# Kernel optimization log

Measured on AMD Instinct MI355X. Metric: run time of the kernel, lower is better.

The kernel has to match this reference:

```python
import jax, jax.numpy as jnp
import numpy as np

N_HEADS = 16


def setup_inputs() -> dict:
    key = jax.random.key(0)
    ks = jax.random.split(key, 4)
    B, S, D = 2, 2048, 1024
    x = jax.random.normal(ks[0], (B, S, D), dtype=jnp.float32)
    scale = 1.0 / np.sqrt(D)
    Wq = jax.random.normal(ks[1], (D, D), dtype=jnp.float32) * scale
    Wk = jax.random.normal(ks[2], (D, D), dtype=jnp.float32) * scale
    Wv = jax.random.normal(ks[3], (D, D), dtype=jnp.float32) * scale
    bq = jnp.zeros((D,), jnp.float32)
    bk = jnp.zeros((D,), jnp.float32)
    bv = jnp.zeros((D,), jnp.float32)
    return {"x": x, "Wq": Wq, "bq": bq, "Wk": Wk, "bk": bk, "Wv": Wv, "bv": bv}


def _split_heads(t, n_heads):
    B, S, D = t.shape
    return t.reshape(B, S, n_heads, D // n_heads).transpose(0, 2, 1, 3)  # [B,H,S,hd]


def reference(x, Wq, bq, Wk, bk, Wv, bv):
    H = N_HEADS
    Q = _split_heads(x @ Wq + bq, H)
    K = _split_heads(x @ Wk + bk, H)
    V = _split_heads(x @ Wv + bv, H)
    head_size = Q.shape[-1]
    scores = jnp.einsum("bhqd,bhkd->bhqk", Q, K) / jnp.sqrt(jnp.float32(head_size))
    probs = jax.nn.softmax(scores, axis=-1)  # dropout p=0.01 -> identity in eval
    out = jnp.einsum("bhqk,bhkd->bhqd", probs, V)
    B, _, S, hd = out.shape
    return out.transpose(0, 2, 1, 3).reshape(B, S, H * hd)
```

## Files before the change

kernel.cpp:

```cpp
#include <hip/hip_runtime.h>
#include <hip/hip_bf16.h>

typedef __bf16 bf16x8 __attribute__((ext_vector_type(8)));
typedef __bf16 bf16x4 __attribute__((ext_vector_type(4)));
typedef float f32x4 __attribute__((ext_vector_type(4)));

#define B_ 2
#define S_ 2048
#define D_ 1024
#define H_ 16
#define HD_ 64
#define NT_ (S_ / 64)

__device__ inline void load_lds16(const __bf16* g, __bf16* l) {
  __builtin_amdgcn_global_load_lds(
      (const __attribute__((address_space(1))) void*)g,
      (__attribute__((address_space(3))) void*)l, 16, 0, 0);
}

__global__ __launch_bounds__(256) void prep(
    const float* __restrict__ X,
    const float* __restrict__ Wq, const float* __restrict__ Wk,
    const float* __restrict__ Wv,
    __bf16* __restrict__ Xb, __bf16* __restrict__ WT)
{
  const int z = blockIdx.z, t = threadIdx.x;
  if (z == 3) {
    size_t base = ((size_t)(blockIdx.y * 16 + blockIdx.x)) * 16384 + t * 4;
#pragma unroll
    for (int i = 0; i < 16; ++i) {
      size_t idx = base + (size_t)i * 1024;
      f32x4 v = *(const f32x4*)(X + idx);
      __bf16 o[4];
#pragma unroll
      for (int j = 0; j < 4; ++j) o[j] = (__bf16)v[j];
      *(ulong1*)(Xb + idx) = *(ulong1*)o;
    }
    return;
  }
  const float* W = (z == 0) ? Wq : (z == 1) ? Wk : Wv;
  __bf16* WTz = WT + (size_t)z * D_ * D_;
  const int k0 = blockIdx.y * 64, n0 = blockIdx.x * 64;

  __shared__ __bf16 T[64 * 72];
  {
    int kl = t >> 2, cg = (t & 3) * 16;
    const float* wp = W + (size_t)(k0 + kl) * D_ + n0 + cg;
    bf16x8 a, b;
#pragma unroll
    for (int j = 0; j < 4; ++j) { a[j] = (__bf16)wp[j];     a[4 + j] = (__bf16)wp[4 + j]; }
#pragma unroll
    for (int j = 0; j < 4; ++j) { b[j] = (__bf16)wp[8 + j]; b[4 + j] = (__bf16)wp[12 + j]; }
    *(bf16x8*)(T + kl * 72 + cg) = a;
    *(bf16x8*)(T + kl * 72 + cg + 8) = b;
  }
  __syncthreads();
  {
    int nl = t >> 2, kc = (t & 3) * 16;
    bf16x8 a, b;
#pragma unroll
    for (int j = 0; j < 8; ++j) a[j] = T[(kc + j) * 72 + nl];
#pragma unroll
    for (int j = 0; j < 8; ++j) b[j] = T[(kc + 8 + j) * 72 + nl];
    __bf16* op = WTz + (size_t)(n0 + nl) * D_ + k0 + kc;
    *(bf16x8*)(op) = a;
    *(bf16x8*)(op + 8) = b;
  }
}

__global__ __launch_bounds__(256) void qkv_gemm(
    const __bf16* __restrict__ Xb, const __bf16* __restrict__ WT,
    const float* __restrict__ bq, const float* __restrict__ bk,
    const float* __restrict__ bv,
    __bf16* __restrict__ Qw, __bf16* __restrict__ Kw, __bf16* __restrict__ VTw)
{
  const int z = blockIdx.z;
  const __bf16* Wz = WT + (size_t)z * D_ * D_;
  const float* bias = (z == 0) ? bq : (z == 1) ? bk : bv;
  __bf16* outp = (z == 0) ? Qw : (z == 1) ? Kw : VTw;
  const float mult = (z == 0) ? 0.125f * 1.44269504088896f : 1.0f;

  const int tid  = threadIdx.x;
  const int wave = tid >> 6, lane = tid & 63, ln = lane & 15, quad = lane >> 4;
  const int m0 = blockIdx.y * 128, n0 = blockIdx.x * 128;
  const int wm = (wave & 1) * 64, wn = (wave >> 1) * 64;

  __shared__ __bf16 Als[128 * 32];
  __shared__ __bf16 Bls[128 * 32];

  f32x4 acc[4][4] = {};

  for (int k0 = 0; k0 < D_; k0 += 32) {
    __syncthreads();
#pragma unroll
    for (int i = 0; i < 2; ++i) {
      int cb = wave * 128 + i * 64;
      int chunk = cb + lane;
      int row = chunk >> 2, c = chunk & 3;
      int gc = c ^ (row & 3);
      load_lds16(Xb + (size_t)(m0 + row) * D_ + k0 + gc * 8, Als + cb * 8);
      load_lds16(Wz + (size_t)(n0 + row) * D_ + k0 + gc * 8, Bls + cb * 8);
    }
    __syncthreads();

    bf16x8 af[4], bfr[4];
    const int dsw = (quad ^ (ln & 3)) * 8;
#pragma unroll
    for (int mt = 0; mt < 4; ++mt)
      af[mt] = *(const bf16x8*)(Als + (wm + mt * 16 + ln) * 32 + dsw);
#pragma unroll
    for (int nt = 0; nt < 4; ++nt)
      bfr[nt] = *(const bf16x8*)(Bls + (wn + nt * 16 + ln) * 32 + dsw);
#pragma unroll
    for (int mt = 0; mt < 4; ++mt)
#pragma unroll
      for (int nt = 0; nt < 4; ++nt)
        acc[mt][nt] = __builtin_amdgcn_mfma_f32_16x16x32_bf16(af[mt], bfr[nt], acc[mt][nt], 0, 0, 0);
  }

#pragma unroll
  for (int nt = 0; nt < 4; ++nt) {
    int n_g = n0 + wn + nt * 16 + ln;
    float bv_ = bias[n_g];
#pragma unroll
    for (int mt = 0; mt < 4; ++mt) {
      if (z < 2) {
#pragma unroll
        for (int r = 0; r < 4; ++r) {
          int m_g = m0 + wm + mt * 16 + quad * 4 + r;
          outp[(size_t)m_g * D_ + n_g] = (__bf16)((acc[mt][nt][r] + bv_) * mult);
        }
      } else {
        int m_g0 = m0 + wm + mt * 16 + quad * 4;
        bf16x4 v4;
#pragma unroll
        for (int r = 0; r < 4; ++r) v4[r] = (__bf16)(acc[mt][nt][r] + bv_);
        *(bf16x4*)(outp + (size_t)(m_g0 >> 11) * D_ * S_ + (size_t)n_g * S_ + (m_g0 & (S_ - 1))) = v4;
      }
    }
  }
}

__global__ __launch_bounds__(256) void attn(
    const __bf16* __restrict__ Q, const __bf16* __restrict__ K,
    const __bf16* __restrict__ VT, float* __restrict__ out)
{
  const int tid  = threadIdx.x;
  const int wave = tid >> 6, lane = tid & 63, ln = lane & 15, quad = lane >> 4;

  const int f = blockIdx.x;
  const int xcd = f & 7, g = f >> 3;
  const int bh = ((g & 3) << 3) | xcd;
  const int qt = g >> 2;
  const int b = bh >> 4, h = bh & 15;
  const int q0 = qt * 128 + wave * 32;

  const __bf16* Qbase = Q + (size_t)(b * S_ + q0) * D_ + h * HD_;
  bf16x8 qb[2][2];
#pragma unroll
  for (int nt = 0; nt < 2; ++nt)
#pragma unroll
    for (int ks = 0; ks < 2; ++ks)
      qb[nt][ks] = *(const bf16x8*)(Qbase + (size_t)(nt * 16 + ln) * D_ + ks * 32 + quad * 8);

  const __bf16* Kh = K + (size_t)b * S_ * D_ + h * HD_;
  const __bf16* Vh = VT + (size_t)(b * D_ + h * HD_) * S_;

  __shared__ __bf16 Kls[2][64 * 64];
  __shared__ __bf16 Vls[2][80 * 64];
  __shared__ __bf16 Pls[4][32 * 64];
  __bf16* Pw = Pls[wave];

  {
    bf16x8 ones;
#pragma unroll
    for (int j = 0; j < 8; ++j) ones[j] = (__bf16)1.0f;
    int buf = tid >> 7, rr = (tid >> 3) & 15, cc = tid & 7;
    *(bf16x8*)(&Vls[buf][(64 + rr) * 64 + cc * 8]) = ones;
  }

  f32x4 acc[2][5] = {};

  const int swl = ln & 7;

  bf16x8 kreg[2], vreg[2];
#pragma unroll
  for (int i = 0; i < 2; ++i) {
    int chunk = i * 256 + tid, row = chunk >> 3, cc = chunk & 7;
    kreg[i] = *(const bf16x8*)(Kh + (size_t)row * D_ + cc * 8);
    vreg[i] = *(const bf16x8*)(Vh + (size_t)row * S_ + cc * 8);
  }

  for (int kt = 0; kt < NT_; ++kt) {
    __bf16* Kb = Kls[kt & 1];
    __bf16* Vb = Vls[kt & 1];
#pragma unroll
    for (int i = 0; i < 2; ++i) {
      int chunk = i * 256 + tid, row = chunk >> 3, cc = chunk & 7;
      int sw = (cc ^ (row & 7)) * 8;
      *(bf16x8*)(Kb + row * 64 + sw) = kreg[i];
      *(bf16x8*)(Vb + row * 64 + sw) = vreg[i];
    }
    if (kt + 1 < NT_) {
#pragma unroll
      for (int i = 0; i < 2; ++i) {
        int chunk = i * 256 + tid, row = chunk >> 3, cc = chunk & 7;
        kreg[i] = *(const bf16x8*)(Kh + (size_t)((kt + 1) * 64 + row) * D_ + cc * 8);
        vreg[i] = *(const bf16x8*)(Vh + (size_t)row * S_ + (kt + 1) * 64 + cc * 8);
      }
    }
    __syncthreads();

    f32x4 st[4][2] = {};
#pragma unroll
    for (int mt = 0; mt < 4; ++mt) {
#pragma unroll
      for (int ks = 0; ks < 2; ++ks) {
        bf16x8 ka = *(const bf16x8*)(Kb + (mt * 16 + ln) * 64 + ((ks * 4 + quad) ^ swl) * 8);
#pragma unroll
        for (int nt = 0; nt < 2; ++nt)
          st[mt][nt] = __builtin_amdgcn_mfma_f32_16x16x32_bf16(ka, qb[nt][ks], st[mt][nt], 0, 0, 0);
      }
    }

#pragma unroll
    for (int mt = 0; mt < 4; ++mt)
#pragma unroll
      for (int nt = 0; nt < 2; ++nt) {
        bf16x4 pk;
#pragma unroll
        for (int r = 0; r < 4; ++r)
          pk[r] = (__bf16)__builtin_amdgcn_exp2f(st[mt][nt][r]);
        *(bf16x4*)(Pw + (nt * 16 + ln) * 64 + ((2 * mt + (quad >> 1)) ^ swl) * 8 + (quad & 1) * 4) = pk;
      }

#pragma unroll
    for (int ks = 0; ks < 2; ++ks) {
      bf16x8 pa[2];
#pragma unroll
      for (int mt = 0; mt < 2; ++mt)
        pa[mt] = *(const bf16x8*)(Pw + (mt * 16 + ln) * 64 + ((ks * 4 + quad) ^ swl) * 8);
#pragma unroll
      for (int dt = 0; dt < 5; ++dt) {
        int vrow = (dt < 4) ? dt * 16 + ln : 64 + ln;
        bf16x8 vb = *(const bf16x8*)(Vb + vrow * 64 + ((ks * 4 + quad) ^ swl) * 8);
#pragma unroll
        for (int mt = 0; mt < 2; ++mt)
          acc[mt][dt] = __builtin_amdgcn_mfma_f32_16x16x32_bf16(pa[mt], vb, acc[mt][dt], 0, 0, 0);
      }
    }
    __syncthreads();
  }

#pragma unroll
  for (int mt = 0; mt < 2; ++mt)
#pragma unroll
    for (int r = 0; r < 4; ++r) {
      float li = 1.0f / acc[mt][4][r];
      float* op = out + (size_t)(b * S_ + q0 + mt * 16 + quad * 4 + r) * D_ + h * HD_;
#pragma unroll
      for (int dt = 0; dt < 4; ++dt)
        op[dt * 16 + ln] = acc[mt][dt][r] * li;
    }
}

extern "C" void kernel_launch(void* const* d_in, const int* in_sizes, int n_in,
                              void* d_out, int out_size, void* d_ws, size_t ws_size,
                              hipStream_t stream) {
  const float* X  = (const float*)d_in[0];
  const float* Wq = (const float*)d_in[1];
  const float* bq = (const float*)d_in[2];
  const float* Wk = (const float*)d_in[3];
  const float* bk = (const float*)d_in[4];
  const float* Wv = (const float*)d_in[5];
  const float* bv = (const float*)d_in[6];

  __bf16* Qw  = (__bf16*)d_ws;
  __bf16* Kw  = Qw  + (size_t)B_ * S_ * D_;
  __bf16* VTw = Kw  + (size_t)B_ * S_ * D_;
  __bf16* Xb  = VTw + (size_t)B_ * S_ * D_;
  __bf16* WT  = Xb  + (size_t)B_ * S_ * D_;
  float* out = (float*)d_out;

  prep<<<dim3(16, 16, 4), 256, 0, stream>>>(X, Wq, Wk, Wv, Xb, WT);
  qkv_gemm<<<dim3(8, 32, 3), 256, 0, stream>>>(Xb, WT, bq, bk, bv, Qw, Kw, VTw);
  attn<<<512, 256, 0, stream>>>(Qw, Kw, VTw, out);
}
```

Measured before the change: 168.9 us.

## Split attention over key dimension with atomic accumulation and normalization pass

Splits the key/value sequence into two halves, doubling the attention grid to 1024 blocks. Each block atomically adds its unnormalized output and softmax denominator into zeroed buffers, and a separate kernel then divides by the denominator. LDS double buffering is dropped for a single buffer with a sync at the top of each iteration, which lowers shared memory use. In exchange it adds two memsets, fp32 atomics on the full output, and an extra pass over the output.

Result: slower. 189.8 us (+12.4%).

```diff
diff --git a/kernel.cpp b/kernel.cpp
--- a/kernel.cpp
+++ b/kernel.cpp
@@ -11,6 +11,8 @@
 #define H_ 16
 #define HD_ 64
 #define NT_ (S_ / 64)
+#define NSPLIT 2
+#define KT_PER (NT_ / NSPLIT)
 
 __device__ inline void load_lds16(const __bf16* g, __bf16* l) {
   __builtin_amdgcn_global_load_lds(
@@ -143,7 +145,8 @@
 
 __global__ __launch_bounds__(256) void attn(
     const __bf16* __restrict__ Q, const __bf16* __restrict__ K,
-    const __bf16* __restrict__ VT, float* __restrict__ out)
+    const __bf16* __restrict__ VT, float* __restrict__ O,
+    float* __restrict__ L)
 {
   const int tid  = threadIdx.x;
   const int wave = tid >> 6, lane = tid & 63, ln = lane & 15, quad = lane >> 4;
@@ -151,9 +154,12 @@
   const int f = blockIdx.x;
   const int xcd = f & 7, g = f >> 3;
   const int bh = ((g & 3) << 3) | xcd;
-  const int qt = g >> 2;
+  const int rest = g >> 2;
+  const int qt = rest & 15;
+  const int sk = rest >> 4;
   const int b = bh >> 4, h = bh & 15;
   const int q0 = qt * 128 + wave * 32;
+  const int kt0 = sk * KT_PER, kt1 = kt0 + KT_PER;
 
   const __bf16* Qbase = Q + (size_t)(b * S_ + q0) * D_ + h * HD_;
   bf16x8 qb[2][2];
@@ -166,42 +172,40 @@
   const __bf16* Kh = K + (size_t)b * S_ * D_ + h * HD_;
   const __bf16* Vh = VT + (size_t)(b * D_ + h * HD_) * S_;
 
-  __shared__ __bf16 Kls[2][64 * 64];
-  __shared__ __bf16 Vls[2][80 * 64];
+  __shared__ __bf16 Kls[64 * 64];
+  __shared__ __bf16 Vls[80 * 64];
   __shared__ __bf16 Pls[4][32 * 64];
   __bf16* Pw = Pls[wave];
 
-  {
+  if (tid < 128) {
     bf16x8 ones;
 #pragma unroll
     for (int j = 0; j < 8; ++j) ones[j] = (__bf16)1.0f;
-    int buf = tid >> 7, rr = (tid >> 3) & 15, cc = tid & 7;
-    *(bf16x8*)(&Vls[buf][(64 + rr) * 64 + cc * 8]) = ones;
+    int rr = tid >> 3, cc = tid & 7;
+    *(bf16x8*)(&Vls[(64 + rr) * 64 + cc * 8]) = ones;
   }
 
   f32x4 acc[2][5] = {};
-
   const int swl = ln & 7;
 
   bf16x8 kreg[2], vreg[2];
 #pragma unroll
   for (int i = 0; i < 2; ++i) {
     int chunk = i * 256 + tid, row = chunk >> 3, cc = chunk & 7;
-    kreg[i] = *(const bf16x8*)(Kh + (size_t)row * D_ + cc * 8);
-    vreg[i] = *(const bf16x8*)(Vh + (size_t)row * S_ + cc * 8);
-  }
-
-  for (int kt = 0; kt < NT_; ++kt) {
-    __bf16* Kb = Kls[kt & 1];
-    __bf16* Vb = Vls[kt & 1];
+    kreg[i] = *(const bf16x8*)(Kh + (size_t)(kt0 * 64 + row) * D_ + cc * 8);
+    vreg[i] = *(const bf16x8*)(Vh + (size_t)row * S_ + kt0 * 64 + cc * 8);
+  }
+
+  for (int kt = kt0; kt < kt1; ++kt) {
+    __syncthreads();
 #pragma unroll
     for (int i = 0; i < 2; ++i) {
       int chunk = i * 256 + tid, row = chunk >> 3, cc = chunk & 7;
       int sw = (cc ^ (row & 7)) * 8;
-      *(bf16x8*)(Kb + row * 64 + sw) = kreg[i];
-      *(bf16x8*)(Vb + row * 64 + sw) = vreg[i];
-    }
-    if (kt + 1 < NT_) {
+      *(bf16x8*)(Kls + row * 64 + sw) = kreg[i];
+      *(bf16x8*)(Vls + row * 64 + sw) = vreg[i];
+    }
+    if (kt + 1 < kt1) {
 #pragma unroll
       for (int i = 0; i < 2; ++i) {
         int chunk = i * 256 + tid, row = chunk >> 3, cc = chunk & 7;
@@ -216,7 +220,7 @@
     for (int mt = 0; mt < 4; ++mt) {
 #pragma unroll
       for (int ks = 0; ks < 2; ++ks) {
-        bf16x8 ka = *(const bf16x8*)(Kb + (mt * 16 + ln) * 64 + ((ks * 4 + quad) ^ swl) * 8);
+        bf16x8 ka = *(const bf16x8*)(Kls + (mt * 16 + ln) * 64 + ((ks * 4 + quad) ^ swl) * 8);
 #pragma unroll
         for (int nt = 0; nt < 2; ++nt)
           st[mt][nt] = __builtin_amdgcn_mfma_f32_16x16x32_bf16(ka, qb[nt][ks], st[mt][nt], 0, 0, 0);
@@ -243,25 +247,44 @@
 #pragma unroll
       for (int dt = 0; dt < 5; ++dt) {
         int vrow = (dt < 4) ? dt * 16 + ln : 64 + ln;
-        bf16x8 vb = *(const bf16x8*)(Vb + vrow * 64 + ((ks * 4 + quad) ^ swl) * 8);
+        bf16x8 vb = *(const bf16x8*)(Vls + vrow * 64 + ((ks * 4 + quad) ^ swl) * 8);
 #pragma unroll
         for (int mt = 0; mt < 2; ++mt)
           acc[mt][dt] = __builtin_amdgcn_mfma_f32_16x16x32_bf16(pa[mt], vb, acc[mt][dt], 0, 0, 0);
       }
     }
-    __syncthreads();
-  }
-
+  }
+
+  if (ln == 0) {
+#pragma unroll
+    for (int mt = 0; mt < 2; ++mt)
+#pragma unroll
+      for (int r = 0; r < 4; ++r)
+        atomicAdd(&L[(size_t)bh * S_ + q0 + mt * 16 + quad * 4 + r], acc[mt][4][r]);
+  }
 #pragma unroll
   for (int mt = 0; mt < 2; ++mt)
 #pragma unroll
     for (int r = 0; r < 4; ++r) {
-      float li = 1.0f / acc[mt][4][r];
-      float* op = out + (size_t)(b * S_ + q0 + mt * 16 + quad * 4 + r) * D_ + h * HD_;
+      float* op = O + (size_t)(b * S_ + q0 + mt * 16 + quad * 4 + r) * D_ + h * HD_;
 #pragma unroll
       for (int dt = 0; dt < 4; ++dt)
-        op[dt * 16 + ln] = acc[mt][dt][r] * li;
-    }
+        atomicAdd(&op[dt * 16 + ln], acc[mt][dt][r]);
+    }
+}
+
+__global__ __launch_bounds__(256) void norm_kernel(float* __restrict__ O,
+                                                   const float* __restrict__ L)
+{
+  int idx = (blockIdx.x * 256 + threadIdx.x) * 4;
+  int col = idx & (D_ - 1);
+  int h = col >> 6;
+  int bs = idx >> 10;
+  int b = bs >> 11, s = bs & (S_ - 1);
+  float linv = 1.0f / L[(size_t)(b * H_ + h) * S_ + s];
+  f32x4 v = *(const f32x4*)(O + idx);
+  v *= linv;
+  *(f32x4*)(O + idx) = v;
 }
 
 extern "C" void kernel_launch(void* const* d_in, const int* in_sizes, int n_in,
@@ -280,9 +303,15 @@
   __bf16* VTw = Kw  + (size_t)B_ * S_ * D_;
   __bf16* Xb  = VTw + (size_t)B_ * S_ * D_;
   __bf16* WT  = Xb  + (size_t)B_ * S_ * D_;
+  float*  Lb  = (float*)(WT + (size_t)3 * D_ * D_);
   float* out = (float*)d_out;
 
   prep<<<dim3(16, 16, 4), 256, 0, stream>>>(X, Wq, Wk, Wv, Xb, WT);
   qkv_gemm<<<dim3(8, 32, 3), 256, 0, stream>>>(Xb, WT, bq, bk, bv, Qw, Kw, VTw);
-  attn<<<512, 256, 0, stream>>>(Qw, Kw, VTw, out);
-}
+
+  hipMemsetAsync(out, 0, (size_t)B_ * S_ * D_ * sizeof(float), stream);
+  hipMemsetAsync(Lb, 0, (size_t)B_ * H_ * S_ * sizeof(float), stream);
+
+  attn<<<1024, 256, 0, stream>>>(Qw, Kw, VTw, out, Lb);
+  norm_kernel<<<(B_ * S_ * D_ / 4) / 256, 256, 0, stream>>>(out, Lb);
+}
```

## Load K/V fragments directly from global into registers, drop shared staging

Applied to the files above, without the earlier changes.

The attention kernel no longer stages K and V tiles through double-buffered shared memory with block-wide barriers. Each wave now loads its MFMA operand fragments straight from global memory into registers, prefetching the next K tile in a ping-pong register set. The row-sum normalizer is no longer computed by an extra ones-row MFMA; it is accumulated from the exp values and reduced with cross-lane shuffles. This removes LDS traffic, the two __syncthreads per tile and the fifth MFMA column. In exchange the four waves each fetch the same K/V separately, so global/L2 traffic rises, and register pressure goes up.

Measured after the change: 231.7 us. 1.37x slower.

```diff
diff --git a/kernel.cpp b/kernel.cpp
--- a/kernel.cpp
+++ b/kernel.cpp
@@ -166,62 +166,47 @@
   const __bf16* Kh = K + (size_t)b * S_ * D_ + h * HD_;
   const __bf16* Vh = VT + (size_t)(b * D_ + h * HD_) * S_;
 
-  __shared__ __bf16 Kls[2][64 * 64];
-  __shared__ __bf16 Vls[2][80 * 64];
   __shared__ __bf16 Pls[4][32 * 64];
+  __shared__ float  Linv[4][32];
   __bf16* Pw = Pls[wave];
 
-  {
-    bf16x8 ones;
-#pragma unroll
-    for (int j = 0; j < 8; ++j) ones[j] = (__bf16)1.0f;
-    int buf = tid >> 7, rr = (tid >> 3) & 15, cc = tid & 7;
-    *(bf16x8*)(&Vls[buf][(64 + rr) * 64 + cc * 8]) = ones;
-  }
-
-  f32x4 acc[2][5] = {};
-
+  f32x4 acc[2][4] = {};
+  float lsum[2] = {0.f, 0.f};
   const int swl = ln & 7;
 
-  bf16x8 kreg[2], vreg[2];
-#pragma unroll
-  for (int i = 0; i < 2; ++i) {
-    int chunk = i * 256 + tid, row = chunk >> 3, cc = chunk & 7;
-    kreg[i] = *(const bf16x8*)(Kh + (size_t)row * D_ + cc * 8);
-    vreg[i] = *(const bf16x8*)(Vh + (size_t)row * S_ + cc * 8);
-  }
-
-  for (int kt = 0; kt < NT_; ++kt) {
-    __bf16* Kb = Kls[kt & 1];
-    __bf16* Vb = Vls[kt & 1];
-#pragma unroll
-    for (int i = 0; i < 2; ++i) {
-      int chunk = i * 256 + tid, row = chunk >> 3, cc = chunk & 7;
-      int sw = (cc ^ (row & 7)) * 8;
-      *(bf16x8*)(Kb + row * 64 + sw) = kreg[i];
-      *(bf16x8*)(Vb + row * 64 + sw) = vreg[i];
+  const __bf16* Kf = Kh + (size_t)ln * D_ + quad * 8;
+  const __bf16* Vf = Vh + (size_t)ln * S_ + quad * 8;
+
+  bf16x8 kaA[8], kaB[8];
+#pragma unroll
+  for (int i = 0; i < 8; ++i) {
+    int mt = i >> 1, ks = i & 1;
+    kaA[i] = *(const bf16x8*)(Kf + (size_t)(mt * 16) * D_ + ks * 32);
+  }
+
+  auto tile = [&](int kt, bf16x8 (&kc)[8], bf16x8 (&kn)[8]) {
+    bf16x8 vb[8];
+#pragma unroll
+    for (int i = 0; i < 8; ++i) {
+      int ks = i >> 2, dt = i & 3;
+      vb[i] = *(const bf16x8*)(Vf + (size_t)(dt * 16) * S_ + kt * 64 + ks * 32);
     }
     if (kt + 1 < NT_) {
 #pragma unroll
-      for (int i = 0; i < 2; ++i) {
-        int chunk = i * 256 + tid, row = chunk >> 3, cc = chunk & 7;
-        kreg[i] = *(const bf16x8*)(Kh + (size_t)((kt + 1) * 64 + row) * D_ + cc * 8);
-        vreg[i] = *(const bf16x8*)(Vh + (size_t)row * S_ + (kt + 1) * 64 + cc * 8);
+      for (int i = 0; i < 8; ++i) {
+        int mt = i >> 1, ks = i & 1;
+        kn[i] = *(const bf16x8*)(Kf + (size_t)((kt + 1) * 64 + mt * 16) * D_ + ks * 32);
       }
     }
-    __syncthreads();
 
     f32x4 st[4][2] = {};
 #pragma unroll
-    for (int mt = 0; mt < 4; ++mt) {
-#pragma unroll
-      for (int ks = 0; ks < 2; ++ks) {
-        bf16x8 ka = *(const bf16x8*)(Kb + (mt * 16 + ln) * 64 + ((ks * 4 + quad) ^ swl) * 8);
+    for (int mt = 0; mt < 4; ++mt)
+#pragma unroll
+      for (int ks = 0; ks < 2; ++ks)
 #pragma unroll
         for (int nt = 0; nt < 2; ++nt)
-          st[mt][nt] = __builtin_amdgcn_mfma_f32_16x16x32_bf16(ka, qb[nt][ks], st[mt][nt], 0, 0, 0);
-      }
-    }
+          st[mt][nt] = __builtin_amdgcn_mfma_f32_16x16x32_bf16(kc[mt * 2 + ks], qb[nt][ks], st[mt][nt], 0, 0, 0);
 
 #pragma unroll
     for (int mt = 0; mt < 4; ++mt)
@@ -229,8 +214,11 @@
       for (int nt = 0; nt < 2; ++nt) {
         bf16x4 pk;
 #pragma unroll
-        for (int r = 0; r < 4; ++r)
-          pk[r] = (__bf16)__builtin_amdgcn_exp2f(st[mt][nt][r]);
+        for (int r = 0; r < 4; ++r) {
+          float p = __builtin_amdgcn_exp2f(st[mt][nt][r]);
+          lsum[nt] += p;
+          pk[r] = (__bf16)p;
+        }
         *(bf16x4*)(Pw + (nt * 16 + ln) * 64 + ((2 * mt + (quad >> 1)) ^ swl) * 8 + (quad & 1) * 4) = pk;
       }
 
@@ -241,22 +229,33 @@
       for (int mt = 0; mt < 2; ++mt)
         pa[mt] = *(const bf16x8*)(Pw + (mt * 16 + ln) * 64 + ((ks * 4 + quad) ^ swl) * 8);
 #pragma unroll
-      for (int dt = 0; dt < 5; ++dt) {
-        int vrow = (dt < 4) ? dt * 16 + ln : 64 + ln;
-        bf16x8 vb = *(const bf16x8*)(Vb + vrow * 64 + ((ks * 4 + quad) ^ swl) * 8);
+      for (int dt = 0; dt < 4; ++dt)
 #pragma unroll
         for (int mt = 0; mt < 2; ++mt)
-          acc[mt][dt] = __builtin_amdgcn_mfma_f32_16x16x32_bf16(pa[mt], vb, acc[mt][dt], 0, 0, 0);
-      }
-    }
-    __syncthreads();
+          acc[mt][dt] = __builtin_amdgcn_mfma_f32_16x16x32_bf16(pa[mt], vb[ks * 4 + dt], acc[mt][dt], 0, 0, 0);
+    }
+  };
+
+  for (int kt = 0; kt < NT_; kt += 2) {
+    tile(kt, kaA, kaB);
+    tile(kt + 1, kaB, kaA);
+  }
+
+#pragma unroll
+  for (int nt = 0; nt < 2; ++nt) {
+    lsum[nt] += __shfl_xor(lsum[nt], 16);
+    lsum[nt] += __shfl_xor(lsum[nt], 32);
+  }
+  if (quad == 0) {
+    Linv[wave][ln]      = 1.0f / lsum[0];
+    Linv[wave][16 + ln] = 1.0f / lsum[1];
   }
 
 #pragma unroll
   for (int mt = 0; mt < 2; ++mt)
 #pragma unroll
     for (int r = 0; r < 4; ++r) {
-      float li = 1.0f / acc[mt][4][r];
+      float li = Linv[wave][mt * 16 + quad * 4 + r];
       float* op = out + (size_t)(b * S_ + q0 + mt * 16 + quad * 4 + r) * D_ + h * HD_;
 #pragma unroll
       for (int dt = 0; dt < 4; ++dt)
```
